# Kernel optimization log

Measured on AMD Instinct MI355X. Metric: run time of the kernel, lower is better.

## Reference

```python
import jax, jax.numpy as jnp
import numpy as np
import math

B, L = 32, 1000
N_CHAR, EMB, D_MODEL, N_HEADS, PRED_HS, N_OUT = 256, 512, 512, 8, 512, 8
D_HEAD = D_MODEL // N_HEADS


def _pos_encoding(seq_len, d_model, dtype=jnp.float32):
    pos = jnp.arange(seq_len, dtype=dtype)[:, None]                      # [L,1]
    div = jnp.exp(jnp.arange(0, d_model, 2, dtype=dtype) * (-math.log(10000.0) / d_model))
    pe = jnp.zeros((seq_len, d_model), dtype=dtype)
    pe = pe.at[:, 0::2].set(jnp.sin(pos * div))
    pe = pe.at[:, 1::2].set(jnp.cos(pos * div))
    return pe                                                            # [L,D]


def setup_inputs() -> dict:
    key = jax.random.key(0)
    ks = jax.random.split(key, 12)
    def xavier(k, shape):
        fan_in, fan_out = shape[1], shape[0]
        lim = math.sqrt(6.0 / (fan_in + fan_out))
        return jax.random.uniform(k, shape, jnp.float32, -lim, lim)
    data = jax.random.randint(ks[0], (B, L), 0, N_CHAR, dtype=jnp.int64)
    lengths = jnp.clip(jax.random.randint(ks[1], (B,), 0, L, dtype=jnp.int64), 1, L)
    emb = jax.random.normal(ks[2], (N_CHAR, EMB), jnp.float32) * math.sqrt(2.0 / (N_CHAR + EMB))
    return {
        'data': data,
        'lengths': lengths,
        'emb': emb,
        'Wq': xavier(ks[3], (D_MODEL, EMB)), 'bq': jnp.zeros((D_MODEL,), jnp.float32),
        'Wk': xavier(ks[4], (D_MODEL, EMB)), 'bk': jnp.zeros((D_MODEL,), jnp.float32),
        'Wv': xavier(ks[5], (D_MODEL, EMB)), 'bv': jnp.zeros((D_MODEL,), jnp.float32),
        'W1': xavier(ks[6], (PRED_HS, D_MODEL)), 'b1': jnp.full((PRED_HS,), 0.01, jnp.float32),
        'W2': xavier(ks[7], (N_OUT, PRED_HS)), 'b2': jnp.full((N_OUT,), 0.01, jnp.float32),
    }


def reference(data, lengths, emb, Wq, bq, Wk, bk, Wv, bv, W1, b1, W2, b2):
    bs, seq = data.shape
    x = emb[data]                                              # [B,L,E]
    x = x + _pos_encoding(seq, x.shape[-1], x.dtype)[None]     # positional encoding
    # q/k/v projections -> [B,L,H,dh]
    q = (x @ Wq.T + bq).reshape(bs, seq, N_HEADS, D_HEAD)
    k = (x @ Wk.T + bk).reshape(bs, seq, N_HEADS, D_HEAD)
    v = (x @ Wv.T + bv).reshape(bs, seq, N_HEADS, D_HEAD)
    scale = 1.0 / math.sqrt(D_HEAD)
    score = jnp.einsum('bqhd,bkhd->bhqk', q, k) * scale        # [B,H,L,L]
    causal = jnp.tril(jnp.ones((seq, seq), dtype=bool))        # True = keep
    score = jnp.where(causal[None, None], score, -jnp.inf)
    attn = jax.nn.softmax(score, axis=-1)
    ctx = jnp.einsum('bhqk,bkhd->bqhd', attn, v).reshape(bs, seq, D_MODEL)
    # take hidden state at last valid position per sequence
    ctx_last = jnp.take_along_axis(ctx, (lengths - 1)[:, None, None].astype(jnp.int32), axis=1)[:, 0]  # [B,D]
    h = jax.nn.leaky_relu(ctx_last @ W1.T + b1)                # pred layer 1
    out = jax.nn.relu(h @ W2.T + b2)                           # [B,8]
    out = jnp.mean(out, axis=-1)                               # [B]
    return jax.nn.leaky_relu(out)
```

## Files before the change

kernel.cpp:

```cpp
#include <hip/hip_runtime.h>
#include <math.h>

#define BATCH   32
#define LSEQ    1000
#define NHEADS  8
#define DHEAD   64
#define PE_C    (-9.210340371976184f / 512.0f)

__device__ __forceinline__ float pe_val(int j, int e) {
  int ef = e & ~1;
  float dv  = __expf((float)ef * PE_C);
  float arg = (float)j * dv;
  return (e & 1) ? __cosf(arg) : __sinf(arg);
}

__global__ __launch_bounds__(256) void qfold_kernel(
    const int* __restrict__ data, const int* __restrict__ lengths,
    const float* __restrict__ emb,
    const float* __restrict__ Wq, const float* __restrict__ bq,
    const float* __restrict__ Wk, const float* __restrict__ bk,
    float* __restrict__ wfT4, float* __restrict__ bias_dot) {
  int h = blockIdx.x, b = blockIdx.y;
  int p = lengths[b] - 1;
  int t = threadIdx.x;
  __shared__ float xs[512];
  __shared__ float red[256];
  __shared__ float qs[64];
  int tok = data[b * LSEQ + p];
  const float* er = emb + (size_t)tok * 512;
  xs[t]       = er[t]       + pe_val(p, t);
  xs[t + 256] = er[t + 256] + pe_val(p, t + 256);
  __syncthreads();
  int col = h * 64 + (t & 63);
  int kp  = t >> 6;
  {
    const float* wr = Wq + (size_t)col * 512 + kp * 128;
    const float* xp = xs + kp * 128;
    float a = 0.0f;
    for (int e = 0; e < 128; e += 4) {
      float4 wv = *(const float4*)(wr + e);
      a += wv.x * xp[e] + wv.y * xp[e + 1] + wv.z * xp[e + 2] + wv.w * xp[e + 3];
    }
    red[t] = a;
  }
  __syncthreads();
  if (t < 64) {
    float qval = (red[t] + red[t + 64] + red[t + 128] + red[t + 192]
                  + bq[h * 64 + t]) * 0.125f;
    qs[t] = qval;
    float bd = qval * bk[h * 64 + t];
    #pragma unroll
    for (int o = 32; o > 0; o >>= 1) bd += __shfl_xor(bd, o, 64);
    if (t == 0) bias_dot[b * NHEADS + h] = bd;
  }
  __syncthreads();
  float a0 = 0.0f, a1 = 0.0f;
  const float* wkb = Wk + (size_t)(h * 64) * 512;
  for (int d = 0; d < 64; ++d) {
    float qd = qs[d];
    a0 += qd * wkb[d * 512 + t];
    a1 += qd * wkb[d * 512 + t + 256];
  }
  int bh = b * NHEADS + h;
  int e1 = t, e2 = t + 256;
  wfT4[(e1 >> 2) * 1024 + bh * 4 + (e1 & 3)] = a0;
  wfT4[(e2 >> 2) * 1024 + bh * 4 + (e2 & 3)] = a1;
}

__global__ __launch_bounds__(256) void foldmd_kernel(
    const float* __restrict__ emb, const float* __restrict__ wfT4,
    const float* __restrict__ bias_dot, float* __restrict__ MD) {
  __shared__ float rows[8 * 512];
  int t   = threadIdx.x;
  int r0  = blockIdx.x * 8;
  int bh0 = blockIdx.y * 64;
  #pragma unroll
  for (int i = 0; i < 4; ++i) {
    int fi = t + i * 256;
    int rr = fi >> 7;
    int e  = (fi & 127) * 4;
    int rg = r0 + rr;
    float4 v;
    if (rg < 256) {
      v = *(const float4*)(emb + (size_t)rg * 512 + e);
    } else {
      int j = rg - 256;
      float dv0 = __expf((float)e * PE_C);
      float dv1 = __expf((float)(e + 2) * PE_C);
      float a0 = (float)j * dv0, a1 = (float)j * dv1;
      v.x = __sinf(a0); v.y = __cosf(a0);
      v.z = __sinf(a1); v.w = __cosf(a1);
    }
    *(float4*)(&rows[rr * 512 + e]) = v;
  }
  __syncthreads();
  int bh_l = t & 63;
  int rp   = t >> 6;
  const float* rw0 = rows + (2 * rp) * 512;
  const float* rw1 = rows + (2 * rp + 1) * 512;
  const float* wp  = wfT4 + (bh0 + bh_l) * 4;
  float a0 = 0.0f, a1 = 0.0f;
  #pragma unroll 8
  for (int g = 0; g < 128; ++g) {
    float4 w4 = *(const float4*)(wp + g * 1024);
    float4 v0 = *(const float4*)(rw0 + 4 * g);
    float4 v1 = *(const float4*)(rw1 + 4 * g);
    a0 += v0.x * w4.x + v0.y * w4.y + v0.z * w4.z + v0.w * w4.w;
    a1 += v1.x * w4.x + v1.y * w4.y + v1.z * w4.z + v1.w * w4.w;
  }
  float bd = (r0 < 256) ? bias_dot[bh0 + bh_l] : 0.0f;
  MD[(size_t)(r0 + 2 * rp)     * 256 + bh0 + bh_l] = a0 + bd;
  MD[(size_t)(r0 + 2 * rp + 1) * 256 + bh0 + bh_l] = a1 + bd;
}

__global__ __launch_bounds__(256) void attn_ypass_kernel(
    const int* __restrict__ data, const int* __restrict__ lengths,
    const float* __restrict__ emb, const float* __restrict__ MD,
    float* __restrict__ mS, float* __restrict__ y_part) {
  int jc = blockIdx.x, b = blockIdx.y;
  int n = lengths[b];
  int j0 = jc * 125;
  if (j0 >= n) return;
  int cnt = min(125, n - j0);
  int t = threadIdx.x;
  __shared__ float sl[125][8];
  __shared__ int   tk[125];
  __shared__ float redw[4][8];
  __shared__ float m_sh[8], s_sh[8];
  const float* Edot = MD;
  const float* Pdot = MD + 256 * 256;
  if (t < 125) {
    if (t < cnt) {
      int tok = data[b * LSEQ + j0 + t];
      tk[t] = tok;
      const float* er = Edot + (size_t)tok * 256 + b * 8;
      const float* pr = Pdot + (size_t)(j0 + t) * 256 + b * 8;
      float4 e0 = *(const float4*)(er);
      float4 e1 = *(const float4*)(er + 4);
      float4 p0 = *(const float4*)(pr);
      float4 p1 = *(const float4*)(pr + 4);
      sl[t][0] = e0.x + p0.x; sl[t][1] = e0.y + p0.y;
      sl[t][2] = e0.z + p0.z; sl[t][3] = e0.w + p0.w;
      sl[t][4] = e1.x + p1.x; sl[t][5] = e1.y + p1.y;
      sl[t][6] = e1.z + p1.z; sl[t][7] = e1.w + p1.w;
    } else {
      #pragma unroll
      for (int h = 0; h < 8; ++h) sl[t][h] = -INFINITY;
    }
  }
  __syncthreads();
  int h = t & 7, jg = t >> 3, w = t >> 6;
  {
    float m = -INFINITY;
    for (int j = jg; j < 125; j += 32) m = fmaxf(m, sl[j][h]);
    #pragma unroll
    for (int o = 8; o < 64; o <<= 1) m = fmaxf(m, __shfl_xor(m, o, 64));
    if ((t & 63) < 8) redw[w][t & 7] = m;
  }
  __syncthreads();
  if (t < 8)
    m_sh[t] = fmaxf(fmaxf(redw[0][t], redw[1][t]),
                    fmaxf(redw[2][t], redw[3][t]));
  __syncthreads();
  {
    float mh = m_sh[h];
    float sum = 0.0f;
    for (int j = jg; j < 125; j += 32) {
      float p = __expf(sl[j][h] - mh);
      sl[j][h] = p;
      sum += p;
    }
    #pragma unroll
    for (int o = 8; o < 64; o <<= 1) sum += __shfl_xor(sum, o, 64);
    if ((t & 63) < 8) redw[w][t & 7] = sum;
  }
  __syncthreads();
  if (t < 8)
    s_sh[t] = redw[0][t] + redw[1][t] + redw[2][t] + redw[3][t];
  __syncthreads();
  int lane = t & 63;
  int e0i = w * 128 + lane * 2;
  float dv = __expf((float)e0i * PE_C);
  float acc0[8] = {0,0,0,0,0,0,0,0};
  float acc1[8] = {0,0,0,0,0,0,0,0};
  for (int jj = 0; jj < cnt; ++jj) {
    int tok = tk[jj];
    float2 ev = *(const float2*)(emb + (size_t)tok * 512 + e0i);
    float arg = (float)(j0 + jj) * dv;
    float x0 = ev.x + __sinf(arg);
    float x1 = ev.y + __cosf(arg);
    #pragma unroll
    for (int hh = 0; hh < 8; ++hh) {
      float pj = sl[jj][hh];
      acc0[hh] += pj * x0;
      acc1[hh] += pj * x1;
    }
  }
  size_t base = (size_t)(b * 8 + jc) * 4096 + e0i;
  #pragma unroll
  for (int hh = 0; hh < 8; ++hh) {
    float2 o; o.x = acc0[hh]; o.y = acc1[hh];
    *(float2*)(y_part + base + hh * 512) = o;
  }
  if (t < 8) {
    float2 ms; ms.x = m_sh[t]; ms.y = s_sh[t];
    *(float2*)(mS + ((size_t)(b * 8 + jc) * 8 + t) * 2) = ms;
  }
}

__global__ __launch_bounds__(256) void ctx_kernel(
    const int* __restrict__ lengths, const float* __restrict__ y_part,
    const float* __restrict__ mS, const float* __restrict__ Wv,
    const float* __restrict__ bv, float* __restrict__ ctx) {
  int h = blockIdx.x, b = blockIdx.y;
  int t = threadIdx.x;
  __shared__ float ys[512];
  __shared__ float red[256];
  int n = lengths[b];
  int nc = (n + 124) / 125;
  float M = -INFINITY;
  for (int jc = 0; jc < nc; ++jc)
    M = fmaxf(M, mS[((size_t)(b * 8 + jc) * 8 + h) * 2]);
  float S = 0.0f, s0 = 0.0f, s1 = 0.0f;
  for (int jc = 0; jc < nc; ++jc) {
    float2 ms = *(const float2*)(mS + ((size_t)(b * 8 + jc) * 8 + h) * 2);
    float wgt = __expf(ms.x - M);
    S += wgt * ms.y;
    size_t base = (size_t)(b * 8 + jc) * 4096 + h * 512;
    s0 += wgt * y_part[base + t];
    s1 += wgt * y_part[base + t + 256];
  }
  float inv = 1.0f / S;
  ys[t]       = s0 * inv;
  ys[t + 256] = s1 * inv;
  __syncthreads();
  int col = h * 64 + (t & 63);
  int kp  = t >> 6;
  const float* wr = Wv + (size_t)col * 512 + kp * 128;
  const float* xp = ys + kp * 128;
  float a = 0.0f;
  for (int e = 0; e < 128; e += 4) {
    float4 wv4 = *(const float4*)(wr + e);
    a += wv4.x * xp[e] + wv4.y * xp[e + 1] + wv4.z * xp[e + 2] + wv4.w * xp[e + 3];
  }
  red[t] = a;
  __syncthreads();
  if (t < 64)
    ctx[b * 512 + h * 64 + t] =
        red[t] + red[t + 64] + red[t + 128] + red[t + 192] + bv[h * 64 + t];
}

__global__ __launch_bounds__(256) void mlp1_kernel(
    const float* __restrict__ ctx, const float* __restrict__ W1,
    const float* __restrict__ b1, float* __restrict__ hs) {
  int chunk = blockIdx.x, b = blockIdx.y;
  int t = threadIdx.x;
  __shared__ float xs[512];
  __shared__ float red[256];
  xs[t]       = ctx[b * 512 + t];
  xs[t + 256] = ctx[b * 512 + t + 256];
  __syncthreads();
  int col = chunk * 64 + (t & 63);
  int kp  = t >> 6;
  const float* wr = W1 + (size_t)col * 512 + kp * 128;
  const float* xp = xs + kp * 128;
  float a = 0.0f;
  for (int e = 0; e < 128; e += 4) {
    float4 wv = *(const float4*)(wr + e);
    a += wv.x * xp[e] + wv.y * xp[e + 1] + wv.z * xp[e + 2] + wv.w * xp[e + 3];
  }
  red[t] = a;
  __syncthreads();
  if (t < 64) {
    float v = red[t] + red[t + 64] + red[t + 128] + red[t + 192] + b1[chunk * 64 + t];
    hs[b * 512 + chunk * 64 + t] = (v > 0.0f) ? v : 0.01f * v;
  }
}

__global__ __launch_bounds__(256) void mlp2_kernel(
    const float* __restrict__ hs, const float* __restrict__ W2,
    const float* __restrict__ b2, float* __restrict__ out) {
  int b = blockIdx.x, t = threadIdx.x;
  __shared__ float o8[8];
  int j = t >> 5, sub = t & 31;
  const float* hr  = hs + (size_t)b * 512;
  const float* w2r = W2 + (size_t)j * 512;
  float part = 0.0f;
  for (int e = sub * 16; e < sub * 16 + 16; e += 4) {
    float4 wv = *(const float4*)(w2r + e);
    float4 hv = *(const float4*)(hr + e);
    part += wv.x * hv.x + wv.y * hv.y + wv.z * hv.z + wv.w * hv.w;
  }
  #pragma unroll
  for (int o = 16; o > 0; o >>= 1) part += __shfl_xor(part, o, 64);
  if (sub == 0) o8[j] = fmaxf(part + b2[j], 0.0f);
  __syncthreads();
  if (t == 0) {
    float m = 0.0f;
    #pragma unroll
    for (int i = 0; i < 8; ++i) m += o8[i];
    m *= 0.125f;
    out[b] = (m > 0.0f) ? m : 0.01f * m;
  }
}

extern "C" void kernel_launch(void* const* d_in, const int* in_sizes, int n_in,
                              void* d_out, int out_size, void* d_ws, size_t ws_size,
                              hipStream_t stream) {
  const int*   data    = (const int*)d_in[0];
  const int*   lengths = (const int*)d_in[1];
  const float* emb     = (const float*)d_in[2];
  const float* Wq      = (const float*)d_in[3];
  const float* bq      = (const float*)d_in[4];
  const float* Wk      = (const float*)d_in[5];
  const float* bk      = (const float*)d_in[6];
  const float* Wv      = (const float*)d_in[7];
  const float* bv      = (const float*)d_in[8];
  const float* W1      = (const float*)d_in[9];
  const float* b1      = (const float*)d_in[10];
  const float* W2      = (const float*)d_in[11];
  const float* b2      = (const float*)d_in[12];
  float* out = (float*)d_out;

  char* ws = (char*)d_ws;
  float* wfT4     = (float*)(ws);
  float* MD       = (float*)(ws + 524288);
  float* bias_dot = (float*)(ws + 1810432);
  float* mS       = (float*)(ws + 1811456);
  float* y_part   = (float*)(ws + 1827840);
  float* ctx      = (float*)(ws + 6022144);
  float* hs       = (float*)(ws + 6087680);

  dim3 g1(NHEADS, BATCH);
  qfold_kernel<<<g1, 256, 0, stream>>>(data, lengths, emb, Wq, bq, Wk, bk,
                                       wfT4, bias_dot);
  dim3 g2(157, 4);
  foldmd_kernel<<<g2, 256, 0, stream>>>(emb, wfT4, bias_dot, MD);
  dim3 g3(8, BATCH);
  attn_ypass_kernel<<<g3, 256, 0, stream>>>(data, lengths, emb, MD, mS, y_part);
  dim3 g4(NHEADS, BATCH);
  ctx_kernel<<<g4, 256, 0, stream>>>(lengths, y_part, mS, Wv, bv, ctx);
  dim3 g5(8, BATCH);
  mlp1_kernel<<<g5, 256, 0, stream>>>(ctx, W1, b1, hs);
  mlp2_kernel<<<BATCH, 256, 0, stream>>>(hs, W2, b2, out);
}
```

Before: 140.9 us.

## Split attention into 64-key chunks and fuse MLP layers with atomic reduction

The attention y-pass now uses 16 chunks of 64 keys per batch instead of 8 chunks of 125. This doubles the number of blocks and shortens the serial per-block loop over keys, at the cost of more partial results for ctx_kernel to merge. The two MLP kernels are merged into one: each block atomically adds its share of the W2 output into a per-batch accumulator, and the last block to finish, found through an atomic counter, applies the final activation. The accumulators are zeroed in the first kernel, which removes one kernel launch and the round trip of the hidden state through memory.

```diff
diff --git a/kernel.cpp b/kernel.cpp
--- a/kernel.cpp
+++ b/kernel.cpp
@@ -19,10 +19,15 @@
     const float* __restrict__ emb,
     const float* __restrict__ Wq, const float* __restrict__ bq,
     const float* __restrict__ Wk, const float* __restrict__ bk,
-    float* __restrict__ wfT4, float* __restrict__ bias_dot) {
+    float* __restrict__ wfT4, float* __restrict__ bias_dot,
+    float* __restrict__ acc2, int* __restrict__ cntb) {
   int h = blockIdx.x, b = blockIdx.y;
   int p = lengths[b] - 1;
   int t = threadIdx.x;
+  if (h == 0) {
+    if (t < 8) acc2[b * 8 + t] = 0.0f;
+    else if (t == 8) cntb[b] = 0;
+  }
   __shared__ float xs[512];
   __shared__ float red[256];
   __shared__ float qs[64];
@@ -119,17 +124,17 @@
     float* __restrict__ mS, float* __restrict__ y_part) {
   int jc = blockIdx.x, b = blockIdx.y;
   int n = lengths[b];
-  int j0 = jc * 125;
+  int j0 = jc * 64;
   if (j0 >= n) return;
-  int cnt = min(125, n - j0);
+  int cnt = min(64, n - j0);
   int t = threadIdx.x;
-  __shared__ float sl[125][8];
-  __shared__ int   tk[125];
+  __shared__ float sl[64][8];
+  __shared__ int   tk[64];
   __shared__ float redw[4][8];
   __shared__ float m_sh[8], s_sh[8];
   const float* Edot = MD;
   const float* Pdot = MD + 256 * 256;
-  if (t < 125) {
+  if (t < 64) {
     if (t < cnt) {
       int tok = data[b * LSEQ + j0 + t];
       tk[t] = tok;
@@ -151,8 +156,7 @@
   __syncthreads();
   int h = t & 7, jg = t >> 3, w = t >> 6;
   {
-    float m = -INFINITY;
-    for (int j = jg; j < 125; j += 32) m = fmaxf(m, sl[j][h]);
+    float m = fmaxf(sl[jg][h], sl[jg + 32][h]);
     #pragma unroll
     for (int o = 8; o < 64; o <<= 1) m = fmaxf(m, __shfl_xor(m, o, 64));
     if ((t & 63) < 8) redw[w][t & 7] = m;
@@ -164,12 +168,11 @@
   __syncthreads();
   {
     float mh = m_sh[h];
-    float sum = 0.0f;
-    for (int j = jg; j < 125; j += 32) {
-      float p = __expf(sl[j][h] - mh);
-      sl[j][h] = p;
-      sum += p;
-    }
+    float p0 = __expf(sl[jg][h] - mh);
+    float p1 = __expf(sl[jg + 32][h] - mh);
+    sl[jg][h] = p0;
+    sl[jg + 32][h] = p1;
+    float sum = p0 + p1;
     #pragma unroll
     for (int o = 8; o < 64; o <<= 1) sum += __shfl_xor(sum, o, 64);
     if ((t & 63) < 8) redw[w][t & 7] = sum;
@@ -196,7 +199,7 @@
       acc1[hh] += pj * x1;
     }
   }
-  size_t base = (size_t)(b * 8 + jc) * 4096 + e0i;
+  size_t base = (size_t)(b * 16 + jc) * 4096 + e0i;
   #pragma unroll
   for (int hh = 0; hh < 8; ++hh) {
     float2 o; o.x = acc0[hh]; o.y = acc1[hh];
@@ -204,7 +207,7 @@
   }
   if (t < 8) {
     float2 ms; ms.x = m_sh[t]; ms.y = s_sh[t];
-    *(float2*)(mS + ((size_t)(b * 8 + jc) * 8 + t) * 2) = ms;
+    *(float2*)(mS + ((size_t)(b * 16 + jc) * 8 + t) * 2) = ms;
   }
 }
 
@@ -217,16 +220,16 @@
   __shared__ float ys[512];
   __shared__ float red[256];
   int n = lengths[b];
-  int nc = (n + 124) / 125;
+  int nc = (n + 63) >> 6;
   float M = -INFINITY;
   for (int jc = 0; jc < nc; ++jc)
-    M = fmaxf(M, mS[((size_t)(b * 8 + jc) * 8 + h) * 2]);
+    M = fmaxf(M, mS[((size_t)(b * 16 + jc) * 8 + h) * 2]);
   float S = 0.0f, s0 = 0.0f, s1 = 0.0f;
   for (int jc = 0; jc < nc; ++jc) {
-    float2 ms = *(const float2*)(mS + ((size_t)(b * 8 + jc) * 8 + h) * 2);
+    float2 ms = *(const float2*)(mS + ((size_t)(b * 16 + jc) * 8 + h) * 2);
     float wgt = __expf(ms.x - M);
     S += wgt * ms.y;
-    size_t base = (size_t)(b * 8 + jc) * 4096 + h * 512;
+    size_t base = (size_t)(b * 16 + jc) * 4096 + h * 512;
     s0 += wgt * y_part[base + t];
     s1 += wgt * y_part[base + t + 256];
   }
@@ -250,13 +253,16 @@
         red[t] + red[t + 64] + red[t + 128] + red[t + 192] + bv[h * 64 + t];
 }
 
-__global__ __launch_bounds__(256) void mlp1_kernel(
+__global__ __launch_bounds__(256) void mlp_kernel(
     const float* __restrict__ ctx, const float* __restrict__ W1,
-    const float* __restrict__ b1, float* __restrict__ hs) {
+    const float* __restrict__ b1, const float* __restrict__ W2,
+    const float* __restrict__ b2, float* __restrict__ acc2,
+    int* __restrict__ cntb, float* __restrict__ out) {
   int chunk = blockIdx.x, b = blockIdx.y;
   int t = threadIdx.x;
   __shared__ float xs[512];
   __shared__ float red[256];
+  __shared__ float hv_sh[64];
   xs[t]       = ctx[b * 512 + t];
   xs[t + 256] = ctx[b * 512 + t + 256];
   __syncthreads();
@@ -272,35 +278,33 @@
   red[t] = a;
   __syncthreads();
   if (t < 64) {
-    float v = red[t] + red[t + 64] + red[t + 128] + red[t + 192] + b1[chunk * 64 + t];
-    hs[b * 512 + chunk * 64 + t] = (v > 0.0f) ? v : 0.01f * v;
-  }
-}
-
-__global__ __launch_bounds__(256) void mlp2_kernel(
-    const float* __restrict__ hs, const float* __restrict__ W2,
-    const float* __restrict__ b2, float* __restrict__ out) {
-  int b = blockIdx.x, t = threadIdx.x;
-  __shared__ float o8[8];
-  int j = t >> 5, sub = t & 31;
-  const float* hr  = hs + (size_t)b * 512;
-  const float* w2r = W2 + (size_t)j * 512;
-  float part = 0.0f;
-  for (int e = sub * 16; e < sub * 16 + 16; e += 4) {
-    float4 wv = *(const float4*)(w2r + e);
-    float4 hv = *(const float4*)(hr + e);
-    part += wv.x * hv.x + wv.y * hv.y + wv.z * hv.z + wv.w * hv.w;
-  }
-  #pragma unroll
-  for (int o = 16; o > 0; o >>= 1) part += __shfl_xor(part, o, 64);
-  if (sub == 0) o8[j] = fmaxf(part + b2[j], 0.0f);
-  __syncthreads();
-  if (t == 0) {
-    float m = 0.0f;
-    #pragma unroll
-    for (int i = 0; i < 8; ++i) m += o8[i];
-    m *= 0.125f;
-    out[b] = (m > 0.0f) ? m : 0.01f * m;
+    float v = red[t] + red[t + 64] + red[t + 128] + red[t + 192] + b1[col];
+    hv_sh[t] = (v > 0.0f) ? v : 0.01f * v;
+  }
+  __syncthreads();
+  if (t < 64) {
+    float hvv = hv_sh[t];
+    #pragma unroll
+    for (int j = 0; j < 8; ++j) {
+      float p = W2[(size_t)j * 512 + col] * hvv;
+      #pragma unroll
+      for (int o = 32; o > 0; o >>= 1) p += __shfl_xor(p, o, 64);
+      if (t == 0) atomicAdd(&acc2[b * 8 + j], p);
+    }
+    if (t == 0) {
+      __threadfence();
+      int old = atomicAdd(&cntb[b], 1);
+      if (old == 7) {
+        float m = 0.0f;
+        #pragma unroll
+        for (int j = 0; j < 8; ++j) {
+          float vj = atomicAdd(&acc2[b * 8 + j], 0.0f) + b2[j];
+          m += fmaxf(vj, 0.0f);
+        }
+        m *= 0.125f;
+        out[b] = (m > 0.0f) ? m : 0.01f * m;
+      }
+    }
   }
 }
 
@@ -327,20 +331,20 @@
   float* MD       = (float*)(ws + 524288);
   float* bias_dot = (float*)(ws + 1810432);
   float* mS       = (float*)(ws + 1811456);
-  float* y_part   = (float*)(ws + 1827840);
-  float* ctx      = (float*)(ws + 6022144);
-  float* hs       = (float*)(ws + 6087680);
+  float* y_part   = (float*)(ws + 1844224);
+  float* ctx      = (float*)(ws + 10232832);
+  float* acc2     = (float*)(ws + 10298368);
+  int*   cntb     = (int*)  (ws + 10299392);
 
   dim3 g1(NHEADS, BATCH);
   qfold_kernel<<<g1, 256, 0, stream>>>(data, lengths, emb, Wq, bq, Wk, bk,
-                                       wfT4, bias_dot);
+                                       wfT4, bias_dot, acc2, cntb);
   dim3 g2(157, 4);
   foldmd_kernel<<<g2, 256, 0, stream>>>(emb, wfT4, bias_dot, MD);
-  dim3 g3(8, BATCH);
+  dim3 g3(16, BATCH);
   attn_ypass_kernel<<<g3, 256, 0, stream>>>(data, lengths, emb, MD, mS, y_part);
   dim3 g4(NHEADS, BATCH);
   ctx_kernel<<<g4, 256, 0, stream>>>(lengths, y_part, mS, Wv, bv, ctx);
   dim3 g5(8, BATCH);
-  mlp1_kernel<<<g5, 256, 0, stream>>>(ctx, W1, b1, hs);
-  mlp2_kernel<<<BATCH, 256, 0, stream>>>(hs, W2, b2, out);
-}
+  mlp_kernel<<<g5, 256, 0, stream>>>(ctx, W1, b1, W2, b2, acc2, cntb, out);
+}
```

Result: slower. 148.5 us (+5.4%).
